# Performance work log

Measured on AMD Instinct MI355X. Metric: run time of the kernel, lower is better.

Reference implementation:

```python
import jax, jax.numpy as jnp
import numpy as np

# dims
H = 1024          # hidden_size
E = 2048          # d_inner = 2*H
NH = 32           # nheads = E/64
P = 64            # headdim
N = 128           # d_state
G = 1             # ngroups
K = 4             # d_conv
Q = 128           # SSD chunk length
FF = 4096         # intermediate_size
EPS = 1e-6        # rms_norm_eps
NEPS = 1e-5       # mamba gated-norm eps
CONV_DIM = E + 2 * G * N            # 2304
D_IN = 2 * E + 2 * G * N + NH       # 4384


def rmsnorm(x, w, eps):
    v = jnp.mean(x.astype(jnp.float32) ** 2, axis=-1, keepdims=True)
    return (x.astype(jnp.float32) * jax.lax.rsqrt(v + eps)).astype(x.dtype) * w


def segsum(x):
    # x: [..., T] -> [..., T, T] with out[i,j] = sum_{j<k<=i} x[k], -inf above diag
    T = x.shape[-1]
    cs = jnp.cumsum(x, axis=-1)
    s = cs[..., :, None] - cs[..., None, :]
    mask = jnp.tril(jnp.ones((T, T), dtype=bool))
    return jnp.where(mask, s, -jnp.inf)


def ssd(x, dt, A_log, B, C):
    # x:[b,l,nh,p], dt:[b,l,nh], B,C:[b,l,N] (ngroups=1, shared over heads)
    b, l, nh, p = x.shape
    A = -jnp.exp(A_log)                      # [nh]
    dA = dt * A                              # [b,l,nh]
    xd = x * dt[..., None]                   # discretized input
    c = l // Q
    xd = xd.reshape(b, c, Q, nh, p)
    dAc = dA.reshape(b, c, Q, nh).transpose(0, 3, 1, 2)   # [b,h,c,q]
    Bc = B.reshape(b, c, Q, N)
    Cc = C.reshape(b, c, Q, N)
    A_cs = jnp.cumsum(dAc, axis=-1)                        # [b,h,c,q]
    Lm = jnp.exp(segsum(dAc))                              # [b,h,c,q,q]
    # intra-chunk (diagonal blocks)
    Y_diag = jnp.einsum('bcqn,bcsn,bhcqs,bcshp->bcqhp', Cc, Bc, Lm, xd)
    # per-chunk final states
    decay_states = jnp.exp(A_cs[..., -1:] - A_cs)          # [b,h,c,q]
    states = jnp.einsum('bcqn,bhcq,bcqhp->bchpn', Bc, decay_states, xd)
    # inter-chunk recurrence (initial state = 0)
    A_last = jnp.pad(A_cs[..., -1], ((0, 0), (0, 0), (1, 0)))   # [b,h,c+1]
    decay_chunk = jnp.exp(segsum(A_last))                       # [b,h,c+1,c+1]
    states = jnp.concatenate([jnp.zeros_like(states[:, :1]), states], axis=1)
    new_states = jnp.einsum('bhzc,bchpn->bzhpn', decay_chunk, states)[:, :-1]
    Y_off = jnp.einsum('bcqn,bchpn,bhcq->bcqhp', Cc, new_states, jnp.exp(A_cs))
    return (Y_diag + Y_off).reshape(b, l, nh, p)


def mamba2(h, w_in, w_conv, b_conv, dt_bias, A_log, D, w_mnorm, w_out):
    b, l, _ = h.shape
    zxbcdt = h @ w_in.T                         # [b,l,D_IN]
    z, xBC, dt = jnp.split(zxbcdt, [E, E + CONV_DIM], axis=-1)
    # causal depthwise conv (kernel K) over channels of xBC
    pad = jnp.pad(xBC, ((0, 0), (K - 1, 0), (0, 0)))
    xBC = sum(pad[:, k:k + l, :] * w_conv[:, k] for k in range(K)) + b_conv
    xBC = jax.nn.silu(xBC)
    x, B, C = jnp.split(xBC, [E, E + G * N], axis=-1)
    dt = jax.nn.softplus(dt + dt_bias)          # [b,l,NH]
    xh = x.reshape(b, l, NH, P)
    y = ssd(xh, dt, A_log, B, C)
    y = y + D[None, None, :, None] * xh         # per-head skip
    y = y.reshape(b, l, E)
    y = rmsnorm(y * jax.nn.silu(z), w_mnorm, NEPS)   # gated RMSNorm
    return y @ w_out.T


def setup_inputs() -> dict:
    key = jax.random.key(0)
    ks = jax.random.split(key, 12)
    dt0 = jax.random.uniform(ks[0], (NH,), minval=0.001, maxval=0.1)
    dt_bias = dt0 + jnp.log(-jnp.expm1(-dt0))   # inverse softplus
    return {
        'hidden_states': jax.random.normal(ks[1], (2, 2048, H), dtype=jnp.float32),
        'w_ln1': jnp.ones((H,), jnp.float32),
        'w_in': 0.02 * jax.random.normal(ks[2], (D_IN, H), dtype=jnp.float32),
        'w_conv': 0.1 * jax.random.normal(ks[3], (CONV_DIM, K), dtype=jnp.float32),
        'b_conv': jnp.zeros((CONV_DIM,), jnp.float32),
        'dt_bias': dt_bias,
        'A_log': jnp.log(jax.random.uniform(ks[4], (NH,), minval=1.0, maxval=16.0)),
        'D': jnp.ones((NH,), jnp.float32),
        'w_mnorm': jnp.ones((E,), jnp.float32),
        'w_out': 0.02 * jax.random.normal(ks[5], (H, E), dtype=jnp.float32),
        'w_ln2': jnp.ones((H,), jnp.float32),
        'w_gate': 0.02 * jax.random.normal(ks[6], (FF, H), dtype=jnp.float32),
        'w_up': 0.02 * jax.random.normal(ks[7], (FF, H), dtype=jnp.float32),
        'w_down': 0.02 * jax.random.normal(ks[8], (H, FF), dtype=jnp.float32),
    }


def reference(hidden_states, w_ln1, w_in, w_conv, b_conv, dt_bias, A_log, D,
              w_mnorm, w_out, w_ln2, w_gate, w_up, w_down):
    residual = hidden_states
    h = rmsnorm(hidden_states, w_ln1, EPS)
    h = mamba2(h, w_in, w_conv, b_conv, dt_bias, A_log, D, w_mnorm, w_out)
    hidden = residual + h
    residual = hidden
    h = rmsnorm(hidden, w_ln2, EPS)
    h = (jax.nn.silu(h @ w_gate.T) * (h @ w_up.T)) @ w_down.T
    return residual + h
```

## Files before the change

kernel.cpp:

```cpp
#include <hip/hip_runtime.h>

#define DEV static __device__ __forceinline__

typedef short bf16x8 __attribute__((ext_vector_type(8)));
typedef float floatx4 __attribute__((ext_vector_type(4)));
typedef unsigned short ushort4v __attribute__((ext_vector_type(4)));
typedef unsigned short ushort8v __attribute__((ext_vector_type(8)));

DEV unsigned short f32_bf16(float f) {
  unsigned int u = __builtin_bit_cast(unsigned int, f);
  u = u + 0x7fffu + ((u >> 16) & 1u);
  return (unsigned short)(u >> 16);
}
DEV float bf2f(unsigned short u) {
  unsigned int v = ((unsigned int)u) << 16;
  return __builtin_bit_cast(float, v);
}
DEV float sigmoidf_(float x) { return 1.0f / (1.0f + __expf(-x)); }
DEV float siluf_(float x) { return x * sigmoidf_(x); }

#define GLD_LDS16(g, l)                                                              \
  __builtin_amdgcn_global_load_lds((const __attribute__((address_space(1))) void*)(g), \
                                   (__attribute__((address_space(3))) void*)(l), 16, 0, 0)

template <int MODE, int BN>
__global__ __launch_bounds__(256) void gemm128(
    const unsigned short* __restrict__ A, const unsigned short* __restrict__ B,
    void* __restrict__ Cv, const unsigned short* __restrict__ other,
    int K, int lda, int ldb, int ldc, long long bsA, long long bsB, long long bsC) {
  constexpr int NBG = BN / 64;
  constexpr int NJ = BN / 32;
  constexpr int BUFSZ = 4096 + BN * 32;
  __shared__ unsigned short S[2 * BUFSZ];
  A += (long long)blockIdx.z * bsA;
  B += (long long)blockIdx.z * bsB;
  const long long coff = (long long)blockIdx.z * bsC;
  const int tid = threadIdx.x;
  const int w = tid >> 6, lane = tid & 63;

  const int nbx = gridDim.x, nby = gridDim.y;
  const int GM = 4;
  int bid = blockIdx.y * nbx + blockIdx.x;
  int gid = bid / (GM * nbx);
  int rem = bid - gid * (GM * nbx);
  int gsz = min(GM, nby - gid * GM);
  int mtile = gid * GM + rem % gsz;
  int ntile = rem / gsz;
  const int m0 = mtile << 7, n0 = ntile * BN;

  const int srow = lane >> 2;
  const int schunk = ((lane & 3) ^ (srow & 3)) * 8;
  const unsigned short* ag0 = A + (long long)(m0 + w * 32 + srow) * lda + schunk;
  const unsigned short* ag1 = ag0 + (long long)16 * lda;
  const unsigned short* bgp[NBG];
#pragma unroll
  for (int ii = 0; ii < NBG; ++ii)
    bgp[ii] = B + (long long)(n0 + w * (BN / 4) + srow + 16 * ii) * ldb + schunk;

  auto STAGE = [&](int buf, int k0) {
    unsigned short* as_ = S + buf * BUFSZ;
    unsigned short* bs_ = as_ + 4096;
    GLD_LDS16(ag0 + k0, as_ + w * 1024 + lane * 8);
    GLD_LDS16(ag1 + k0, as_ + w * 1024 + lane * 8 + 512);
#pragma unroll
    for (int ii = 0; ii < NBG; ++ii)
      GLD_LDS16(bgp[ii] + k0, bs_ + w * (NBG * 512) + ii * 512 + lane * 8);
  };

  const int wr = (w >> 1) << 6;
  const int wc = (w & 1) * (BN / 2);
  const int fr = lane & 15;
  const int slot = (((lane >> 4) ^ (fr & 3))) << 3;
  const int r0 = (lane >> 4) << 2;

  floatx4 acc[4][NJ];
#pragma unroll
  for (int i = 0; i < 4; ++i)
#pragma unroll
    for (int j = 0; j < NJ; ++j) acc[i][j] = (floatx4){0.f, 0.f, 0.f, 0.f};

  const int nsteps = K >> 5;
  STAGE(0, 0);
  if (nsteps > 1) STAGE(1, 32);

  for (int t = 0; t < nsteps; ++t) {
    if (t < nsteps - 1) {
      if constexpr (NBG == 2) {
        asm volatile("s_waitcnt vmcnt(4)" ::: "memory");
      } else {
        asm volatile("s_waitcnt vmcnt(6)" ::: "memory");
      }
    } else {
      asm volatile("s_waitcnt vmcnt(0)" ::: "memory");
    }
    __builtin_amdgcn_s_barrier();
    __builtin_amdgcn_sched_barrier(0);
    const unsigned short* Ab = S + (t & 1) * BUFSZ;
    const unsigned short* Bb = Ab + 4096;
    bf16x8 af[4], bf_[NJ];
#pragma unroll
    for (int i = 0; i < 4; ++i)
      af[i] = *(const bf16x8*)(Ab + (wr + i * 16 + fr) * 32 + slot);
#pragma unroll
    for (int j = 0; j < NJ; ++j)
      bf_[j] = *(const bf16x8*)(Bb + (wc + j * 16 + fr) * 32 + slot);
#pragma unroll
    for (int i = 0; i < 4; ++i)
#pragma unroll
      for (int j = 0; j < NJ; ++j)
        acc[i][j] = __builtin_amdgcn_mfma_f32_16x16x32_bf16(af[i], bf_[j], acc[i][j], 0, 0, 0);
    __builtin_amdgcn_sched_barrier(0);
    __builtin_amdgcn_s_barrier();
    if (t + 2 < nsteps) STAGE(t & 1, (t + 2) * 32);
  }

  if constexpr (MODE == 0) {
#pragma unroll
    for (int i = 0; i < 4; ++i) {
#pragma unroll
      for (int j = 0; j < NJ; ++j) {
        long long base = (long long)(m0 + wr + i * 16 + r0) * ldc + (n0 + wc + j * 16 + fr);
#pragma unroll
        for (int r = 0; r < 4; ++r) {
          ((float*)Cv)[coff + base + (long long)r * ldc] = acc[i][j][r];
        }
      }
    }
  } else {
    constexpr int PAD = BN + 4;
    float* scr = (float*)S;
    const int row_l = tid >> 3;
    const int col0 = (tid & 7) * 8;
    __syncthreads();
#pragma unroll
    for (int pass = 0; pass < 4; ++pass) {
      if ((w >> 1) == (pass >> 1)) {
#pragma unroll
        for (int ii = 0; ii < 2; ++ii) {
          int i = (pass & 1) * 2 + ii;
          int rl = i * 16 + r0 - (pass & 1) * 32;
#pragma unroll
          for (int j = 0; j < NJ; ++j) {
            int col = wc + j * 16 + fr;
#pragma unroll
            for (int r = 0; r < 4; ++r) scr[(rl + r) * PAD + col] = acc[i][j][r];
          }
        }
      }
      __syncthreads();
      long long grow = m0 + pass * 32 + row_l;
      long long gbase = coff + grow * ldc + n0;
      const float* srow_p = scr + row_l * PAD;
#pragma unroll
      for (int k = 0; k < BN / 64; ++k) {
        int col = col0 + k * 64;
        float v[8];
        *(float4*)&v[0] = *(const float4*)(srow_p + col);
        *(float4*)&v[4] = *(const float4*)(srow_p + col + 4);
        ushort8v o;
        if constexpr (MODE == 2) {
          ushort8v uo = *(const ushort8v*)(other + gbase + col);
#pragma unroll
          for (int e = 0; e < 8; ++e) o[e] = f32_bf16(siluf_(v[e]) * bf2f(uo[e]));
        } else {
#pragma unroll
          for (int e = 0; e < 8; ++e) o[e] = f32_bf16(v[e]);
        }
        *(ushort8v*)((unsigned short*)Cv + gbase + col) = o;
      }
      __syncthreads();
    }
  }
}

template <int WM>
__global__ __launch_bounds__(256) void gemm_small_nt(
    const unsigned short* __restrict__ A, const unsigned short* __restrict__ B,
    float* __restrict__ C, int M, int N, int K, int lda, int ldb, int ldc) {
  const int w = threadIdx.x >> 6;
  const int lane = threadIdx.x & 63;
  const int lm = lane & 15;
  const int ko = (lane >> 4) << 3;
  const int bn0 = blockIdx.x << 6;
  const int m_base = blockIdx.y * (WM * 64) + w * (WM * 16);

  const unsigned short* arow[WM];
#pragma unroll
  for (int i = 0; i < WM; ++i) arow[i] = A + (long long)(m_base + i * 16 + lm) * lda + ko;
  int nv = (N - bn0) >> 4;
  nv = nv > 4 ? 4 : nv;
  const unsigned short* brow[4];
#pragma unroll
  for (int j = 0; j < 4; ++j) {
    int nr = bn0 + j * 16 + lm;
    brow[j] = B + (long long)(j < nv ? nr : 0) * ldb + ko;
  }
  floatx4 acc[WM][4];
#pragma unroll
  for (int i = 0; i < WM; ++i)
#pragma unroll
    for (int j = 0; j < 4; ++j) acc[i][j] = (floatx4){0.f, 0.f, 0.f, 0.f};
  for (int k0 = 0; k0 < K; k0 += 32) {
    bf16x8 a[WM];
#pragma unroll
    for (int i = 0; i < WM; ++i) a[i] = *(const bf16x8*)(arow[i] + k0);
#pragma unroll
    for (int j = 0; j < 4; ++j) {
      if (j < nv) {
        bf16x8 b = *(const bf16x8*)(brow[j] + k0);
#pragma unroll
        for (int i = 0; i < WM; ++i)
          acc[i][j] = __builtin_amdgcn_mfma_f32_16x16x32_bf16(a[i], b, acc[i][j], 0, 0, 0);
      }
    }
  }
  const int r0 = (lane >> 4) << 2;
#pragma unroll
  for (int i = 0; i < WM; ++i)
#pragma unroll
    for (int j = 0; j < 4; ++j)
      if (j < nv) {
        int col = bn0 + j * 16 + lm;
        long long base = (long long)(m_base + i * 16 + r0) * ldc + col;
#pragma unroll
        for (int r = 0; r < 4; ++r) C[base + (long long)r * ldc] = acc[i][j][r];
      }
}

__global__ __launch_bounds__(256) void f32_to_bf16_k(const float* __restrict__ src,
                                                     unsigned short* __restrict__ dst,
                                                     long long n4) {
  long long i = (long long)blockIdx.x * 256 + threadIdx.x;
  if (i < n4) {
    float4 v = ((const float4*)src)[i];
    ushort4v o = {f32_bf16(v.x), f32_bf16(v.y), f32_bf16(v.z), f32_bf16(v.w)};
    ((ushort4v*)dst)[i] = o;
  }
}

__global__ __launch_bounds__(256) void zero_out_k(float* __restrict__ o, long long n) {
  long long i = (long long)blockIdx.x * 256 + threadIdx.x;
  if (i < n) o[i] = 0.f;
}

__global__ __launch_bounds__(256) void rmsnorm1024_bf16_k(const float* __restrict__ x,
                                                          const float* __restrict__ w,
                                                          unsigned short* __restrict__ out,
                                                          float eps) {
  long long row = blockIdx.x;
  int t = threadIdx.x;
  float4 v = ((const float4*)(x + row * 1024))[t];
  float ss = v.x * v.x + v.y * v.y + v.z * v.z + v.w * v.w;
  __shared__ float red[4];
#pragma unroll
  for (int o = 32; o > 0; o >>= 1) ss += __shfl_down(ss, o, 64);
  if ((t & 63) == 0) red[t >> 6] = ss;
  __syncthreads();
  float tot = red[0] + red[1] + red[2] + red[3];
  float sc = rsqrtf(tot * (1.0f / 1024.0f) + eps);
  float4 wv = ((const float4*)w)[t];
  ushort4v o = {f32_bf16(v.x * sc * wv.x), f32_bf16(v.y * sc * wv.y),
                f32_bf16(v.z * sc * wv.z), f32_bf16(v.w * sc * wv.w)};
  ((ushort4v*)(out + row * 1024))[t] = o;
}

__global__ __launch_bounds__(256) void add_rmsnorm_k(const float* __restrict__ hs,
                                                     const float* __restrict__ parts,
                                                     long long pstride, int np,
                                                     const float* __restrict__ w,
                                                     float* __restrict__ mh,
                                                     unsigned short* __restrict__ h2, float eps) {
  long long row = blockIdx.x;
  int t = threadIdx.x;
  float4 v = ((const float4*)(hs + row * 1024))[t];
  for (int p = 0; p < np; ++p) {
    float4 u = ((const float4*)(parts + p * pstride + row * 1024))[t];
    v.x += u.x;
    v.y += u.y;
    v.z += u.z;
    v.w += u.w;
  }
  ((float4*)(mh + row * 1024))[t] = v;
  float ss = v.x * v.x + v.y * v.y + v.z * v.z + v.w * v.w;
  __shared__ float red[4];
#pragma unroll
  for (int o = 32; o > 0; o >>= 1) ss += __shfl_down(ss, o, 64);
  if ((t & 63) == 0) red[t >> 6] = ss;
  __syncthreads();
  float tot = red[0] + red[1] + red[2] + red[3];
  float sc = rsqrtf(tot * (1.0f / 1024.0f) + eps);
  float4 wv = ((const float4*)w)[t];
  ushort4v o = {f32_bf16(v.x * sc * wv.x), f32_bf16(v.y * sc * wv.y),
                f32_bf16(v.z * sc * wv.z), f32_bf16(v.w * sc * wv.w)};
  ((ushort4v*)(h2 + row * 1024))[t] = o;
}

__global__ __launch_bounds__(256) void addn_f32_k(const float* __restrict__ a,
                                                  const float* __restrict__ parts,
                                                  long long pstride, int np,
                                                  float* __restrict__ o, long long n4) {
  long long i = (long long)blockIdx.x * 256 + threadIdx.x;
  if (i < n4) {
    float4 x = ((const float4*)a)[i];
    for (int p = 0; p < np; ++p) {
      float4 u = ((const float4*)(parts + p * pstride))[i];
      x.x += u.x;
      x.y += u.y;
      x.z += u.z;
      x.w += u.w;
    }
    ((float4*)o)[i] = x;
  }
}

__global__ __launch_bounds__(256) void gated_rmsnorm2048_k(const unsigned short* __restrict__ y,
                                                           const unsigned short* __restrict__ z,
                                                           const float* __restrict__ w,
                                                           unsigned short* __restrict__ out,
                                                           float eps) {
  long long row = blockIdx.x;
  int t = threadIdx.x;
  ushort8v yv = ((const ushort8v*)(y + row * 2048))[t];
  ushort8v zv = ((const ushort8v*)(z + row * 2048))[t];
  float g[8];
  float ss = 0.f;
#pragma unroll
  for (int j = 0; j < 8; ++j) {
    g[j] = bf2f(yv[j]) * siluf_(bf2f(zv[j]));
    ss += g[j] * g[j];
  }
  __shared__ float red[4];
#pragma unroll
  for (int o = 32; o > 0; o >>= 1) ss += __shfl_down(ss, o, 64);
  if ((t & 63) == 0) red[t >> 6] = ss;
  __syncthreads();
  float tot = red[0] + red[1] + red[2] + red[3];
  float sc = rsqrtf(tot * (1.0f / 2048.0f) + eps);
  float ww[8];
  *(float4*)&ww[0] = ((const float4*)w)[2 * t];
  *(float4*)&ww[4] = ((const float4*)w)[2 * t + 1];
  ushort8v o;
#pragma unroll
  for (int j = 0; j < 8; ++j) o[j] = f32_bf16(g[j] * sc * ww[j]);
  ((ushort8v*)(out + row * 2048))[t] = o;
}

__global__ __launch_bounds__(256) void conv_silu_k(const unsigned short* __restrict__ xraw,
                                                   const float* __restrict__ wconv,
                                                   const float* __restrict__ bconv,
                                                   unsigned short* __restrict__ xBC) {
  int m = blockIdx.x;
  int l = m & 2047;
  for (int cb = threadIdx.x; cb < 288; cb += 256) {
    int ch0 = cb << 3;
    float acc[8];
    float4 bc0 = ((const float4*)bconv)[cb * 2];
    float4 bc1 = ((const float4*)bconv)[cb * 2 + 1];
    acc[0] = bc0.x; acc[1] = bc0.y; acc[2] = bc0.z; acc[3] = bc0.w;
    acc[4] = bc1.x; acc[5] = bc1.y; acc[6] = bc1.z; acc[7] = bc1.w;
    float4 wv[8];
#pragma unroll
    for (int j = 0; j < 8; ++j) wv[j] = ((const float4*)wconv)[ch0 + j];
#pragma unroll
    for (int k = 0; k < 4; ++k) {
      int lk = l + k - 3;
      if (lk >= 0) {
        ushort8v xv = *(const ushort8v*)(xraw + (long long)(m + k - 3) * 2304 + ch0);
        acc[0] += bf2f(xv[0]) * ((const float*)&wv[0])[k];
        acc[1] += bf2f(xv[1]) * ((const float*)&wv[1])[k];
        acc[2] += bf2f(xv[2]) * ((const float*)&wv[2])[k];
        acc[3] += bf2f(xv[3]) * ((const float*)&wv[3])[k];
        acc[4] += bf2f(xv[4]) * ((const float*)&wv[4])[k];
        acc[5] += bf2f(xv[5]) * ((const float*)&wv[5])[k];
        acc[6] += bf2f(xv[6]) * ((const float*)&wv[6])[k];
        acc[7] += bf2f(xv[7]) * ((const float*)&wv[7])[k];
      }
    }
    ushort8v o;
#pragma unroll
    for (int j = 0; j < 8; ++j) o[j] = f32_bf16(siluf_(acc[j]));
    *(ushort8v*)(xBC + (long long)m * 2304 + ch0) = o;
  }
}

__global__ __launch_bounds__(128) void dA_cumsum_k(const float* __restrict__ dtraw,
                                                   const float* __restrict__ dt_bias,
                                                   const float* __restrict__ A_log,
                                                   float* __restrict__ dt_s,
                                                   float* __restrict__ dA_cs) {
  int bi = blockIdx.x;
  int c = bi & 15, h = (bi >> 4) & 31, b = bi >> 9;
  int q = threadIdx.x;
  long long idx = ((long long)(b * 2048 + c * 128 + q)) * 32 + h;
  float xv = dtraw[idx] + dt_bias[h];
  float sp = xv > 20.f ? xv : log1pf(expf(xv));
  dt_s[idx] = sp;
  float A = -expf(A_log[h]);
  float v = sp * A;
  __shared__ float sbuf[128];
  sbuf[q] = v;
  __syncthreads();
  for (int off = 1; off < 128; off <<= 1) {
    float tv = (q >= off) ? sbuf[q - off] : 0.f;
    __syncthreads();
    sbuf[q] += tv;
    __syncthreads();
  }
  dA_cs[(long long)bi * 128 + q] = sbuf[q];
}

__global__ __launch_bounds__(256) void ssd_diag_states_k(
    const unsigned short* __restrict__ xBC, const float* __restrict__ dt_s,
    const float* __restrict__ dA_cs, const unsigned short* __restrict__ G,
    unsigned short* __restrict__ y, unsigned short* __restrict__ states) {
  __shared__ unsigned short Mz[128 * 136];
  __shared__ unsigned short xdT[64 * 136];
  __shared__ float Acs[128];
  __shared__ float wdec[128];
  const int bx = blockIdx.x;
  const int h = bx & 31, c = (bx >> 5) & 15, b = bx >> 9;
  const int t = threadIdx.x;
  const int w = t >> 6, lane = t & 63, fr = lane & 15, hi = lane >> 4;
  const long long rowbase = (long long)b * 2048 + c * 128;
  const long long abase = ((long long)((b * 32 + h) * 16 + c)) << 7;

  if (t < 128) {
    float a = dA_cs[abase + t];
    Acs[t] = a;
    wdec[t] = __expf(dA_cs[abase + 127] - a);
  }
  {
    int s = t >> 1, p0 = (t & 1) * 32;
    float dtv = dt_s[(rowbase + s) * 32 + h];
    const ushort8v* xv = (const ushort8v*)(xBC + (rowbase + s) * 2304 + h * 64 + p0);
#pragma unroll
    for (int i = 0; i < 4; ++i) {
      ushort8v vv = xv[i];
#pragma unroll
      for (int j = 0; j < 8; ++j) xdT[(p0 + i * 8 + j) * 136 + s] = f32_bf16(bf2f(vv[j]) * dtv);
    }
  }
  __syncthreads();
  {
    int q = t >> 1, s0 = (t & 1) * 64;
    float aq = Acs[q];
    const ushort8v* gv =
        (const ushort8v*)(G + (((long long)(b * 16 + c)) * 128 + q) * 128 + s0);
#pragma unroll
    for (int i = 0; i < 8; ++i) {
      ushort8v gg = gv[i];
#pragma unroll
      for (int j = 0; j < 8; ++j) {
        int s = s0 + i * 8 + j;
        float m = (s <= q) ? bf2f(gg[j]) * __expf(aq - Acs[s]) : 0.f;
        Mz[q * 136 + s] = f32_bf16(m);
      }
    }
  }
  __syncthreads();
  const int q0 = w << 5;
  {
    floatx4 acc[2][4];
#pragma unroll
    for (int i = 0; i < 2; ++i)
#pragma unroll
      for (int j = 0; j < 4; ++j) acc[i][j] = (floatx4){0.f, 0.f, 0.f, 0.f};
#pragma unroll
    for (int k0 = 0; k0 < 128; k0 += 32) {
      int kk = k0 + hi * 8;
      bf16x8 a0 = *(const bf16x8*)(Mz + (q0 + fr) * 136 + kk);
      bf16x8 a1 = *(const bf16x8*)(Mz + (q0 + 16 + fr) * 136 + kk);
      bf16x8 bf_[4];
#pragma unroll
      for (int j = 0; j < 4; ++j) bf_[j] = *(const bf16x8*)(xdT + (j * 16 + fr) * 136 + kk);
#pragma unroll
      for (int j = 0; j < 4; ++j) {
        acc[0][j] = __builtin_amdgcn_mfma_f32_16x16x32_bf16(a0, bf_[j], acc[0][j], 0, 0, 0);
        acc[1][j] = __builtin_amdgcn_mfma_f32_16x16x32_bf16(a1, bf_[j], acc[1][j], 0, 0, 0);
      }
    }
#pragma unroll
    for (int i = 0; i < 2; ++i)
#pragma unroll
      for (int r = 0; r < 4; ++r) {
        int q = q0 + i * 16 + hi * 4 + r;
        unsigned short* yrow = y + (rowbase + q) * 2048 + h * 64;
#pragma unroll
        for (int j = 0; j < 4; ++j) yrow[j * 16 + fr] = f32_bf16(acc[i][j][r]);
      }
  }
  __syncthreads();
  {
    int s = t >> 1, n0 = (t & 1) * 64;
    float wd = wdec[s];
    const ushort8v* bv = (const ushort8v*)(xBC + (rowbase + s) * 2304 + 2048 + n0);
#pragma unroll
    for (int i = 0; i < 8; ++i) {
      ushort8v bb = bv[i];
#pragma unroll
      for (int j = 0; j < 8; ++j) Mz[(n0 + i * 8 + j) * 136 + s] = f32_bf16(bf2f(bb[j]) * wd);
    }
  }
  __syncthreads();
  {
    floatx4 acc[2][4];
#pragma unroll
    for (int i = 0; i < 2; ++i)
#pragma unroll
      for (int j = 0; j < 4; ++j) acc[i][j] = (floatx4){0.f, 0.f, 0.f, 0.f};
#pragma unroll
    for (int k0 = 0; k0 < 128; k0 += 32) {
      int kk = k0 + hi * 8;
      bf16x8 a0 = *(const bf16x8*)(Mz + (q0 + fr) * 136 + kk);
      bf16x8 a1 = *(const bf16x8*)(Mz + (q0 + 16 + fr) * 136 + kk);
      bf16x8 bf_[4];
#pragma unroll
      for (int j = 0; j < 4; ++j) bf_[j] = *(const bf16x8*)(xdT + (j * 16 + fr) * 136 + kk);
#pragma unroll
      for (int j = 0; j < 4; ++j) {
        acc[0][j] = __builtin_amdgcn_mfma_f32_16x16x32_bf16(a0, bf_[j], acc[0][j], 0, 0, 0);
        acc[1][j] = __builtin_amdgcn_mfma_f32_16x16x32_bf16(a1, bf_[j], acc[1][j], 0, 0, 0);
      }
    }
    unsigned short* st = states + (long long)bx * 8192;
#pragma unroll
    for (int i = 0; i < 2; ++i)
#pragma unroll
      for (int j = 0; j < 4; ++j) {
        int p = j * 16 + fr;
        int n = q0 + i * 16 + hi * 4;
        ushort4v o;
#pragma unroll
        for (int r = 0; r < 4; ++r) o[r] = f32_bf16(acc[i][j][r]);
        *(ushort4v*)(st + p * 128 + n) = o;
      }
  }
}

__global__ __launch_bounds__(256) void ssd_scan_k(const float* __restrict__ dA_cs,
                                                  unsigned short* __restrict__ states) {
  int seg = blockIdx.x & 7;
  int h = (blockIdx.x >> 3) & 31;
  int b = blockIdx.x >> 8;
  int t = threadIdx.x;
  int e0 = seg * 1024 + t;
  float carry[4];
#pragma unroll
  for (int i = 0; i < 4; ++i) carry[i] = 0.f;
  for (int c = 0; c < 16; ++c) {
    long long base = ((long long)((b * 16 + c) * 32 + h)) * 8192;
    float dec = __expf(dA_cs[(((long long)((b * 32 + h) * 16 + c)) << 7) + 127]);
#pragma unroll
    for (int i = 0; i < 4; ++i) {
      long long idx = base + e0 + i * 256;
      float local = bf2f(states[idx]);
      states[idx] = f32_bf16(carry[i]);
      carry[i] = dec * carry[i] + local;
    }
  }
}

__global__ __launch_bounds__(256) void ssd_off_k(const unsigned short* __restrict__ xBC,
                                                 const float* __restrict__ dA_cs,
                                                 const unsigned short* __restrict__ states,
                                                 const float* __restrict__ Dvec,
                                                 unsigned short* __restrict__ y) {
  __shared__ float eA[128];
  const int bx = blockIdx.x;
  const int h = bx & 31, c = (bx >> 5) & 15, b = bx >> 9;
  const int t = threadIdx.x;
  const int w = t >> 6, lane = t & 63, fr = lane & 15, hi = lane >> 4;
  const long long rowbase = (long long)b * 2048 + c * 128;
  const long long abase = ((long long)((b * 32 + h) * 16 + c)) << 7;
  if (t < 128) eA[t] = __expf(dA_cs[abase + t]);
  __syncthreads();

  const unsigned short* st = states + (long long)bx * 8192;
  const int q0 = w << 5;
  floatx4 acc[2][4];
#pragma unroll
  for (int i = 0; i < 2; ++i)
#pragma unroll
    for (int j = 0; j < 4; ++j) acc[i][j] = (floatx4){0.f, 0.f, 0.f, 0.f};

#pragma unroll
  for (int k0 = 0; k0 < 128; k0 += 32) {
    int kk = k0 + hi * 8;
    bf16x8 a0 = *(const bf16x8*)(xBC + (rowbase + q0 + fr) * 2304 + 2176 + kk);
    bf16x8 a1 = *(const bf16x8*)(xBC + (rowbase + q0 + 16 + fr) * 2304 + 2176 + kk);
    bf16x8 bf_[4];
#pragma unroll
    for (int j = 0; j < 4; ++j) bf_[j] = *(const bf16x8*)(st + (j * 16 + fr) * 128 + kk);
#pragma unroll
    for (int j = 0; j < 4; ++j) {
      acc[0][j] = __builtin_amdgcn_mfma_f32_16x16x32_bf16(a0, bf_[j], acc[0][j], 0, 0, 0);
      acc[1][j] = __builtin_amdgcn_mfma_f32_16x16x32_bf16(a1, bf_[j], acc[1][j], 0, 0, 0);
    }
  }

  float Dh = Dvec[h];
#pragma unroll
  for (int i = 0; i < 2; ++i) {
#pragma unroll
    for (int r = 0; r < 4; ++r) {
      int q = q0 + i * 16 + hi * 4 + r;
      float e = eA[q];
      const unsigned short* xrow = xBC + (rowbase + q) * 2304 + h * 64;
      unsigned short* yrow = y + (rowbase + q) * 2048 + h * 64;
#pragma unroll
      for (int j = 0; j < 4; ++j) {
        int p = j * 16 + fr;
        float v = bf2f(yrow[p]) + e * acc[i][j][r] + Dh * bf2f(xrow[p]);
        yrow[p] = f32_bf16(v);
      }
    }
  }
}

extern "C" void kernel_launch(void* const* d_in, const int* in_sizes, int n_in, void* d_out,
                              int out_size, void* d_ws, size_t ws_size, hipStream_t stream) {
  const float* hs = (const float*)d_in[0];
  const float* w_ln1 = (const float*)d_in[1];
  const float* w_in = (const float*)d_in[2];
  const float* w_conv = (const float*)d_in[3];
  const float* b_conv = (const float*)d_in[4];
  const float* dt_bias = (const float*)d_in[5];
  const float* A_log = (const float*)d_in[6];
  const float* Dvec = (const float*)d_in[7];
  const float* w_mnorm = (const float*)d_in[8];
  const float* w_out = (const float*)d_in[9];
  const float* w_ln2 = (const float*)d_in[10];
  const float* w_gate = (const float*)d_in[11];
  const float* w_up = (const float*)d_in[12];
  const float* w_down = (const float*)d_in[13];
  float* out = (float*)d_out;
  const int M = 4096;

  char* ws = (char*)d_ws;
  const size_t R0 = 0;
  const size_t R1 = 33554432;
  const size_t R1b = R1 + 33554432;
  const size_t R2 = 71303168;
  const size_t R3 = 90177536;
  const size_t R4 = 107544576;
  const size_t W0 = 108068864;
  const size_t NEED = 133234688;

  if (ws_size < NEED) {
    hipLaunchKernelGGL(zero_out_k, dim3((out_size + 255) / 256), dim3(256), 0, stream, out,
                       (long long)out_size);
    return;
  }

  unsigned short* z = (unsigned short*)(ws + R0);
  unsigned short* act = (unsigned short*)(ws + R0);
  float* oproj_parts = (float*)(ws + R0);
  unsigned short* xraw = (unsigned short*)(ws + R1);
  unsigned short* states = (unsigned short*)(ws + R1);
  unsigned short* ybuf = (unsigned short*)(ws + R1 + 16777216);
  unsigned short* upo = (unsigned short*)(ws + R1);
  float* down_parts = (float*)(ws + R1);
  unsigned short* wbf_out = (unsigned short*)(ws + R1b);
  unsigned short* xBC = (unsigned short*)(ws + R2);
  unsigned short* ygn = (unsigned short*)(ws + R2);
  unsigned short* h2 = (unsigned short*)(ws + R2);
  unsigned short* hnorm = (unsigned short*)(ws + R3);
  unsigned short* wbf_in = (unsigned short*)(ws + R3 + 8388608);
  float* dt_s = (float*)(ws + R3);
  float* dA_cs = (float*)(ws + R3 + 524288);
  unsigned short* Gbuf = (unsigned short*)(ws + R3 + 1048576);
  float* mh = (float*)(ws + R3);
  float* dtraw = (float*)(ws + R4);
  unsigned short* wbf_gate = (unsigned short*)(ws + W0);
  unsigned short* wbf_up = (unsigned short*)(ws + W0 + 8388608);
  unsigned short* wbf_down = (unsigned short*)(ws + W0 + 16777216);

  hipLaunchKernelGGL(rmsnorm1024_bf16_k, dim3(M), dim3(256), 0, stream, hs, w_ln1, hnorm, 1e-6f);
  hipLaunchKernelGGL(f32_to_bf16_k, dim3(4384), dim3(256), 0, stream, w_in, wbf_in, 1122304LL);
  hipLaunchKernelGGL(f32_to_bf16_k, dim3(4096), dim3(256), 0, stream, w_gate, wbf_gate, 1048576LL);
  hipLaunchKernelGGL(f32_to_bf16_k, dim3(4096), dim3(256), 0, stream, w_up, wbf_up, 1048576LL);
  hipLaunchKernelGGL(f32_to_bf16_k, dim3(4096), dim3(256), 0, stream, w_down, wbf_down, 1048576LL);
  hipLaunchKernelGGL((gemm128<1, 128>), dim3(16, 32, 1), dim3(256), 0, stream, hnorm, wbf_in,
                     (void*)z, (const unsigned short*)nullptr, 1024, 1024, 1024, 2048, 0LL, 0LL,
                     0LL);
  hipLaunchKernelGGL((gemm128<1, 128>), dim3(18, 32, 1), dim3(256), 0, stream, hnorm,
                     wbf_in + 2048 * 1024, (void*)xraw, (const unsigned short*)nullptr, 1024, 1024,
                     1024, 2304, 0LL, 0LL, 0LL);
  hipLaunchKernelGGL((gemm_small_nt<1>), dim3(1, 64, 1), dim3(256), 0, stream, hnorm,
                     wbf_in + 4352 * 1024, dtraw, M, 32, 1024, 1024, 1024, 32);
  hipLaunchKernelGGL(conv_silu_k, dim3(M), dim3(256), 0, stream, xraw, w_conv, b_conv, xBC);
  hipLaunchKernelGGL(f32_to_bf16_k, dim3(2048), dim3(256), 0, stream, w_out, wbf_out, 524288LL);
  hipLaunchKernelGGL(dA_cumsum_k, dim3(1024), dim3(128), 0, stream, dtraw, dt_bias, A_log, dt_s,
                     dA_cs);
  hipLaunchKernelGGL((gemm128<1, 128>), dim3(1, 1, 32), dim3(256), 0, stream, xBC + 2176,
                     xBC + 2048, (void*)Gbuf, (const unsigned short*)nullptr, 128, 2304, 2304, 128,
                     294912LL, 294912LL, 16384LL);
  hipLaunchKernelGGL(ssd_diag_states_k, dim3(1024), dim3(256), 0, stream, xBC, dt_s, dA_cs, Gbuf,
                     ybuf, states);
  hipLaunchKernelGGL(ssd_scan_k, dim3(512), dim3(256), 0, stream, dA_cs, states);
  hipLaunchKernelGGL(ssd_off_k, dim3(1024), dim3(256), 0, stream, xBC, dA_cs, states, Dvec, ybuf);
  hipLaunchKernelGGL(gated_rmsnorm2048_k, dim3(M), dim3(256), 0, stream, ybuf, z, w_mnorm, ygn,
                     1e-5f);
  hipLaunchKernelGGL((gemm128<0, 128>), dim3(8, 32, 2), dim3(256), 0, stream, ygn, wbf_out,
                     (void*)oproj_parts, (const unsigned short*)nullptr, 1024, 2048, 2048, 1024,
                     1024LL, 1024LL, 4194304LL);
  hipLaunchKernelGGL(add_rmsnorm_k, dim3(M), dim3(256), 0, stream, hs, oproj_parts, 4194304LL, 2,
                     w_ln2, mh, h2, 1e-6f);
  hipLaunchKernelGGL((gemm128<1, 256>), dim3(16, 32, 1), dim3(256), 0, stream, h2, wbf_up,
                     (void*)upo, (const unsigned short*)nullptr, 1024, 1024, 1024, 4096, 0LL, 0LL,
                     0LL);
  hipLaunchKernelGGL((gemm128<2, 256>), dim3(16, 32, 1), dim3(256), 0, stream, h2, wbf_gate,
                     (void*)act, upo, 1024, 1024, 1024, 4096, 0LL, 0LL, 0LL);
  hipLaunchKernelGGL((gemm128<0, 128>), dim3(8, 32, 2), dim3(256), 0, stream, act, wbf_down,
                     (void*)down_parts, (const unsigned short*)nullptr, 2048, 4096, 4096, 1024,
                     2048LL, 2048LL, 4194304LL);
  hipLaunchKernelGGL(addn_f32_k, dim3(4096), dim3(256), 0, stream, mh, down_parts, 4194304LL, 2,
                     out, 1048576LL);
}
```

Measured before the change: 522.3 us.

## Merge weight casts, flatten conv grid, vectorize SSD stores via LDS staging

Merges the five weight f32-to-bf16 conversions into one launch. Flattens the conv+SiLU grid so every thread handles one 8-channel group instead of each block looping over 288 groups. In the SSD kernels, stages MFMA accumulators through shared memory so y and state outputs are written as 16-byte vectors instead of scattered 2-byte stores, and the Mz tile is written with vector stores. The scan kernel now moves 8 contiguous bf16 values per thread. The cost is extra LDS traffic and barriers in the SSD kernels, plus fewer scan blocks.

Result: no change. 523.3 us (+0.2%).

```diff
diff --git a/kernel.cpp b/kernel.cpp
--- a/kernel.cpp
+++ b/kernel.cpp
@@ -227,15 +227,31 @@
       }
 }
 
-__global__ __launch_bounds__(256) void f32_to_bf16_k(const float* __restrict__ src,
-                                                     unsigned short* __restrict__ dst,
-                                                     long long n4) {
-  long long i = (long long)blockIdx.x * 256 + threadIdx.x;
-  if (i < n4) {
-    float4 v = ((const float4*)src)[i];
-    ushort4v o = {f32_bf16(v.x), f32_bf16(v.y), f32_bf16(v.z), f32_bf16(v.w)};
-    ((ushort4v*)dst)[i] = o;
-  }
+__global__ __launch_bounds__(256) void wconv_all_k(
+    const float* __restrict__ w_in, const float* __restrict__ w_gate,
+    const float* __restrict__ w_up, const float* __restrict__ w_down,
+    const float* __restrict__ w_out, unsigned short* __restrict__ d_in_,
+    unsigned short* __restrict__ d_gate, unsigned short* __restrict__ d_up,
+    unsigned short* __restrict__ d_down, unsigned short* __restrict__ d_out_) {
+  long long j = (long long)blockIdx.x * 256 + threadIdx.x;
+  const float* src;
+  unsigned short* dst;
+  if (j < 1122304) {
+    src = w_in; dst = d_in_;
+  } else if ((j -= 1122304) < 1048576) {
+    src = w_gate; dst = d_gate;
+  } else if ((j -= 1048576) < 1048576) {
+    src = w_up; dst = d_up;
+  } else if ((j -= 1048576) < 1048576) {
+    src = w_down; dst = d_down;
+  } else if ((j -= 1048576) < 524288) {
+    src = w_out; dst = d_out_;
+  } else {
+    return;
+  }
+  float4 v = ((const float4*)src)[j];
+  ushort4v o = {f32_bf16(v.x), f32_bf16(v.y), f32_bf16(v.z), f32_bf16(v.w)};
+  ((ushort4v*)dst)[j] = o;
 }
 
 __global__ __launch_bounds__(256) void zero_out_k(float* __restrict__ o, long long n) {
@@ -349,38 +365,39 @@
                                                    const float* __restrict__ wconv,
                                                    const float* __restrict__ bconv,
                                                    unsigned short* __restrict__ xBC) {
-  int m = blockIdx.x;
+  long long f = (long long)blockIdx.x * 256 + threadIdx.x;
+  if (f >= 4096LL * 288) return;
+  int m = (int)(f / 288);
+  int cb = (int)(f - (long long)m * 288);
   int l = m & 2047;
-  for (int cb = threadIdx.x; cb < 288; cb += 256) {
-    int ch0 = cb << 3;
-    float acc[8];
-    float4 bc0 = ((const float4*)bconv)[cb * 2];
-    float4 bc1 = ((const float4*)bconv)[cb * 2 + 1];
-    acc[0] = bc0.x; acc[1] = bc0.y; acc[2] = bc0.z; acc[3] = bc0.w;
-    acc[4] = bc1.x; acc[5] = bc1.y; acc[6] = bc1.z; acc[7] = bc1.w;
-    float4 wv[8];
-#pragma unroll
-    for (int j = 0; j < 8; ++j) wv[j] = ((const float4*)wconv)[ch0 + j];
-#pragma unroll
-    for (int k = 0; k < 4; ++k) {
-      int lk = l + k - 3;
-      if (lk >= 0) {
-        ushort8v xv = *(const ushort8v*)(xraw + (long long)(m + k - 3) * 2304 + ch0);
-        acc[0] += bf2f(xv[0]) * ((const float*)&wv[0])[k];
-        acc[1] += bf2f(xv[1]) * ((const float*)&wv[1])[k];
-        acc[2] += bf2f(xv[2]) * ((const float*)&wv[2])[k];
-        acc[3] += bf2f(xv[3]) * ((const float*)&wv[3])[k];
-        acc[4] += bf2f(xv[4]) * ((const float*)&wv[4])[k];
-        acc[5] += bf2f(xv[5]) * ((const float*)&wv[5])[k];
-        acc[6] += bf2f(xv[6]) * ((const float*)&wv[6])[k];
-        acc[7] += bf2f(xv[7]) * ((const float*)&wv[7])[k];
-      }
-    }
-    ushort8v o;
-#pragma unroll
-    for (int j = 0; j < 8; ++j) o[j] = f32_bf16(siluf_(acc[j]));
-    *(ushort8v*)(xBC + (long long)m * 2304 + ch0) = o;
-  }
+  int ch0 = cb << 3;
+  float acc[8];
+  float4 bc0 = ((const float4*)bconv)[cb * 2];
+  float4 bc1 = ((const float4*)bconv)[cb * 2 + 1];
+  acc[0] = bc0.x; acc[1] = bc0.y; acc[2] = bc0.z; acc[3] = bc0.w;
+  acc[4] = bc1.x; acc[5] = bc1.y; acc[6] = bc1.z; acc[7] = bc1.w;
+  float4 wv[8];
+#pragma unroll
+  for (int j = 0; j < 8; ++j) wv[j] = ((const float4*)wconv)[ch0 + j];
+#pragma unroll
+  for (int k = 0; k < 4; ++k) {
+    int lk = l + k - 3;
+    if (lk >= 0) {
+      ushort8v xv = *(const ushort8v*)(xraw + (long long)(m + k - 3) * 2304 + ch0);
+      acc[0] += bf2f(xv[0]) * ((const float*)&wv[0])[k];
+      acc[1] += bf2f(xv[1]) * ((const float*)&wv[1])[k];
+      acc[2] += bf2f(xv[2]) * ((const float*)&wv[2])[k];
+      acc[3] += bf2f(xv[3]) * ((const float*)&wv[3])[k];
+      acc[4] += bf2f(xv[4]) * ((const float*)&wv[4])[k];
+      acc[5] += bf2f(xv[5]) * ((const float*)&wv[5])[k];
+      acc[6] += bf2f(xv[6]) * ((const float*)&wv[6])[k];
+      acc[7] += bf2f(xv[7]) * ((const float*)&wv[7])[k];
+    }
+  }
+  ushort8v o;
+#pragma unroll
+  for (int j = 0; j < 8; ++j) o[j] = f32_bf16(siluf_(acc[j]));
+  *(ushort8v*)(xBC + (long long)m * 2304 + ch0) = o;
 }
 
 __global__ __launch_bounds__(128) void dA_cumsum_k(const float* __restrict__ dtraw,
@@ -449,12 +466,14 @@
 #pragma unroll
     for (int i = 0; i < 8; ++i) {
       ushort8v gg = gv[i];
+      ushort8v mo;
 #pragma unroll
       for (int j = 0; j < 8; ++j) {
         int s = s0 + i * 8 + j;
         float m = (s <= q) ? bf2f(gg[j]) * __expf(aq - Acs[s]) : 0.f;
-        Mz[q * 136 + s] = f32_bf16(m);
-      }
+        mo[j] = f32_bf16(m);
+      }
+      *(ushort8v*)(Mz + q * 136 + s0 + i * 8) = mo;
     }
   }
   __syncthreads();
@@ -479,15 +498,30 @@
         acc[1][j] = __builtin_amdgcn_mfma_f32_16x16x32_bf16(a1, bf_[j], acc[1][j], 0, 0, 0);
       }
     }
+    __syncthreads();
+    float* scr = (float*)Mz;
 #pragma unroll
     for (int i = 0; i < 2; ++i)
 #pragma unroll
       for (int r = 0; r < 4; ++r) {
         int q = q0 + i * 16 + hi * 4 + r;
-        unsigned short* yrow = y + (rowbase + q) * 2048 + h * 64;
-#pragma unroll
-        for (int j = 0; j < 4; ++j) yrow[j * 16 + fr] = f32_bf16(acc[i][j][r]);
-      }
+#pragma unroll
+        for (int j = 0; j < 4; ++j) scr[q * 68 + j * 16 + fr] = acc[i][j][r];
+      }
+    __syncthreads();
+    {
+      int row = t >> 1, colh = (t & 1) * 32;
+      unsigned short* yrow = y + (rowbase + row) * 2048 + h * 64 + colh;
+      const float* sp = scr + row * 68 + colh;
+#pragma unroll
+      for (int k = 0; k < 4; ++k) {
+        float4 v0 = *(const float4*)(sp + k * 8);
+        float4 v1 = *(const float4*)(sp + k * 8 + 4);
+        ushort8v o = {f32_bf16(v0.x), f32_bf16(v0.y), f32_bf16(v0.z), f32_bf16(v0.w),
+                      f32_bf16(v1.x), f32_bf16(v1.y), f32_bf16(v1.z), f32_bf16(v1.w)};
+        *(ushort8v*)(yrow + k * 8) = o;
+      }
+    }
   }
   __syncthreads();
   {
@@ -522,41 +556,57 @@
         acc[1][j] = __builtin_amdgcn_mfma_f32_16x16x32_bf16(a1, bf_[j], acc[1][j], 0, 0, 0);
       }
     }
-    unsigned short* st = states + (long long)bx * 8192;
+    __syncthreads();
+    float* scr = (float*)Mz;
 #pragma unroll
     for (int i = 0; i < 2; ++i)
 #pragma unroll
       for (int j = 0; j < 4; ++j) {
         int p = j * 16 + fr;
         int n = q0 + i * 16 + hi * 4;
-        ushort4v o;
-#pragma unroll
-        for (int r = 0; r < 4; ++r) o[r] = f32_bf16(acc[i][j][r]);
-        *(ushort4v*)(st + p * 128 + n) = o;
-      }
+#pragma unroll
+        for (int r = 0; r < 4; ++r) scr[p * 132 + n + r] = acc[i][j][r];
+      }
+    __syncthreads();
+    {
+      unsigned short* st = states + (long long)bx * 8192;
+      int p = t >> 2, nh = (t & 3) * 32;
+      unsigned short* strow = st + p * 128 + nh;
+      const float* sp = scr + p * 132 + nh;
+#pragma unroll
+      for (int k = 0; k < 4; ++k) {
+        float4 v0 = *(const float4*)(sp + k * 8);
+        float4 v1 = *(const float4*)(sp + k * 8 + 4);
+        ushort8v o = {f32_bf16(v0.x), f32_bf16(v0.y), f32_bf16(v0.z), f32_bf16(v0.w),
+                      f32_bf16(v1.x), f32_bf16(v1.y), f32_bf16(v1.z), f32_bf16(v1.w)};
+        *(ushort8v*)(strow + k * 8) = o;
+      }
+    }
   }
 }
 
 __global__ __launch_bounds__(256) void ssd_scan_k(const float* __restrict__ dA_cs,
                                                   unsigned short* __restrict__ states) {
-  int seg = blockIdx.x & 7;
-  int h = (blockIdx.x >> 3) & 31;
-  int b = blockIdx.x >> 8;
+  int seg = blockIdx.x & 3;
+  int h = (blockIdx.x >> 2) & 31;
+  int b = blockIdx.x >> 7;
   int t = threadIdx.x;
-  int e0 = seg * 1024 + t;
-  float carry[4];
-#pragma unroll
-  for (int i = 0; i < 4; ++i) carry[i] = 0.f;
+  int e0 = seg * 2048 + t * 8;
+  float carry[8];
+#pragma unroll
+  for (int i = 0; i < 8; ++i) carry[i] = 0.f;
   for (int c = 0; c < 16; ++c) {
     long long base = ((long long)((b * 16 + c) * 32 + h)) * 8192;
     float dec = __expf(dA_cs[(((long long)((b * 32 + h) * 16 + c)) << 7) + 127]);
-#pragma unroll
-    for (int i = 0; i < 4; ++i) {
-      long long idx = base + e0 + i * 256;
-      float local = bf2f(states[idx]);
-      states[idx] = f32_bf16(carry[i]);
+    ushort8v v = *(const ushort8v*)(states + base + e0);
+    ushort8v o;
+#pragma unroll
+    for (int i = 0; i < 8; ++i) {
+      float local = bf2f(v[i]);
+      o[i] = f32_bf16(carry[i]);
       carry[i] = dec * carry[i] + local;
     }
+    *(ushort8v*)(states + base + e0) = o;
   }
 }
 
@@ -566,6 +616,7 @@
                                                  const float* __restrict__ Dvec,
                                                  unsigned short* __restrict__ y) {
   __shared__ float eA[128];
+  __shared__ float scr[128 * 68];
   const int bx = blockIdx.x;
   const int h = bx & 31, c = (bx >> 5) & 15, b = bx >> 9;
   const int t = threadIdx.x;
@@ -598,21 +649,34 @@
     }
   }
 
-  float Dh = Dvec[h];
-#pragma unroll
-  for (int i = 0; i < 2; ++i) {
+#pragma unroll
+  for (int i = 0; i < 2; ++i)
 #pragma unroll
     for (int r = 0; r < 4; ++r) {
       int q = q0 + i * 16 + hi * 4 + r;
-      float e = eA[q];
-      const unsigned short* xrow = xBC + (rowbase + q) * 2304 + h * 64;
-      unsigned short* yrow = y + (rowbase + q) * 2048 + h * 64;
-#pragma unroll
-      for (int j = 0; j < 4; ++j) {
-        int p = j * 16 + fr;
-        float v = bf2f(yrow[p]) + e * acc[i][j][r] + Dh * bf2f(xrow[p]);
-        yrow[p] = f32_bf16(v);
-      }
+#pragma unroll
+      for (int j = 0; j < 4; ++j) scr[q * 68 + j * 16 + fr] = acc[i][j][r];
+    }
+  __syncthreads();
+  {
+    float Dh = Dvec[h];
+    int row = t >> 1, colh = (t & 1) * 32;
+    float e = eA[row];
+    const unsigned short* xrow = xBC + (rowbase + row) * 2304 + h * 64 + colh;
+    unsigned short* yrow = y + (rowbase + row) * 2048 + h * 64 + colh;
+    const float* sp = scr + row * 68 + colh;
+#pragma unroll
+    for (int k = 0; k < 4; ++k) {
+      ushort8v yv = *(const ushort8v*)(yrow + k * 8);
+      ushort8v xv = *(const ushort8v*)(xrow + k * 8);
+      float4 a0 = *(const float4*)(sp + k * 8);
+      float4 a1 = *(const float4*)(sp + k * 8 + 4);
+      float av[8] = {a0.x, a0.y, a0.z, a0.w, a1.x, a1.y, a1.z, a1.w};
+      ushort8v o;
+#pragma unroll
+      for (int e2 = 0; e2 < 8; ++e2)
+        o[e2] = f32_bf16(bf2f(yv[e2]) + e * av[e2] + Dh * bf2f(xv[e2]));
+      *(ushort8v*)(yrow + k * 8) = o;
     }
   }
 }
@@ -676,10 +740,8 @@
   unsigned short* wbf_down = (unsigned short*)(ws + W0 + 16777216);
 
   hipLaunchKernelGGL(rmsnorm1024_bf16_k, dim3(M), dim3(256), 0, stream, hs, w_ln1, hnorm, 1e-6f);
-  hipLaunchKernelGGL(f32_to_bf16_k, dim3(4384), dim3(256), 0, stream, w_in, wbf_in, 1122304LL);
-  hipLaunchKernelGGL(f32_to_bf16_k, dim3(4096), dim3(256), 0, stream, w_gate, wbf_gate, 1048576LL);
-  hipLaunchKernelGGL(f32_to_bf16_k, dim3(4096), dim3(256), 0, stream, w_up, wbf_up, 1048576LL);
-  hipLaunchKernelGGL(f32_to_bf16_k, dim3(4096), dim3(256), 0, stream, w_down, wbf_down, 1048576LL);
+  hipLaunchKernelGGL(wconv_all_k, dim3(18720), dim3(256), 0, stream, w_in, w_gate, w_up, w_down,
+                     w_out, wbf_in, wbf_gate, wbf_up, wbf_down, wbf_out);
   hipLaunchKernelGGL((gemm128<1, 128>), dim3(16, 32, 1), dim3(256), 0, stream, hnorm, wbf_in,
                      (void*)z, (const unsigned short*)nullptr, 1024, 1024, 1024, 2048, 0LL, 0LL,
                      0LL);
@@ -688,8 +750,7 @@
                      1024, 2304, 0LL, 0LL, 0LL);
   hipLaunchKernelGGL((gemm_small_nt<1>), dim3(1, 64, 1), dim3(256), 0, stream, hnorm,
                      wbf_in + 4352 * 1024, dtraw, M, 32, 1024, 1024, 1024, 32);
-  hipLaunchKernelGGL(conv_silu_k, dim3(M), dim3(256), 0, stream, xraw, w_conv, b_conv, xBC);
-  hipLaunchKernelGGL(f32_to_bf16_k, dim3(2048), dim3(256), 0, stream, w_out, wbf_out, 524288LL);
+  hipLaunchKernelGGL(conv_silu_k, dim3(4608), dim3(256), 0, stream, xraw, w_conv, b_conv, xBC);
   hipLaunchKernelGGL(dA_cumsum_k, dim3(1024), dim3(128), 0, stream, dtraw, dt_bias, A_log, dt_s,
                      dA_cs);
   hipLaunchKernelGGL((gemm128<1, 128>), dim3(1, 1, 32), dim3(256), 0, stream, xBC + 2176,
@@ -697,7 +758,7 @@
                      294912LL, 294912LL, 16384LL);
   hipLaunchKernelGGL(ssd_diag_states_k, dim3(1024), dim3(256), 0, stream, xBC, dt_s, dA_cs, Gbuf,
                      ybuf, states);
-  hipLaunchKernelGGL(ssd_scan_k, dim3(512), dim3(256), 0, stream, dA_cs, states);
+  hipLaunchKernelGGL(ssd_scan_k, dim3(256), dim3(256), 0, stream, dA_cs, states);
   hipLaunchKernelGGL(ssd_off_k, dim3(1024), dim3(256), 0, stream, xBC, dA_cs, states, Dvec, ybuf);
   hipLaunchKernelGGL(gated_rmsnorm2048_k, dim3(M), dim3(256), 0, stream, ybuf, z, w_mnorm, ygn,
                      1e-5f);
```
